# Performance work log

Measured on AMD Instinct MI355X. Metric: run time of the kernel, lower is better.

## Reference

```python
import jax, jax.numpy as jnp
import numpy as np

N_NODES = 50000
N_EDGES = 800000
D_FEAT = 128
D_EMB = 128


def setup_inputs() -> dict:
    key = jax.random.key(0)
    k1, k2, k3, k4, k5 = jax.random.split(key, 5)
    feature = jax.random.normal(k1, (N_NODES, D_FEAT), dtype=jnp.float32)
    edge_src = jax.random.randint(k2, (N_EDGES,), 0, N_NODES, dtype=jnp.int32)
    edge_dst = jax.random.randint(k3, (N_EDGES,), 0, N_NODES, dtype=jnp.int32)
    edge_w = jax.random.uniform(k4, (N_EDGES,), dtype=jnp.float32)
    # reset_parameters: uniform(-stdv, stdv), stdv = 1/sqrt(embedding_size)
    stdv = 1.0 / np.sqrt(D_EMB)
    weight = jax.random.uniform(k5, (D_FEAT, D_EMB), dtype=jnp.float32,
                                minval=-stdv, maxval=stdv)
    return {"feature": feature, "edge_src": edge_src, "edge_dst": edge_dst,
            "edge_w": edge_w, "weight": weight}


def reference(feature, edge_src, edge_dst, edge_w, weight):
    # spmm(adj, feature): out[dst] += w * feature[src]
    msgs = edge_w[:, None] * feature[edge_src]          # [E, D_FEAT]
    agg = jax.ops.segment_sum(msgs, edge_dst, num_segments=feature.shape[0])
    # residual blend then dense projection
    blended = 0.5 * agg + 0.5 * feature                  # [N, D_FEAT]
    return blended @ weight                              # [N, D_EMB]
```

## Files before the change

### kernel.cpp

```cpp
#include <hip/hip_runtime.h>

#define N_NODES 50000
#define N_EDGES 800000
#define D 128
#define NBUCK 196
#define CAP 4800
#define CHUNK 4096
#define PA_BLKS ((N_EDGES + CHUNK - 1) / CHUNK)
#define FB_BLKS 3125
#define WT_BLKS 16
#define GSTRIDE 16

typedef __attribute__((ext_vector_type(8))) short short8;
typedef __attribute__((ext_vector_type(4))) float f32x4;

__device__ __forceinline__ unsigned short f2bf(float f) {
    unsigned u = __float_as_uint(f);
    u += 0x7fff + ((u >> 16) & 1);
    return (unsigned short)(u >> 16);
}
__device__ __forceinline__ float lo16f(unsigned u) { return __uint_as_float(u << 16); }
__device__ __forceinline__ float hi16f(unsigned u) { return __uint_as_float(u & 0xffff0000u); }

__global__ __launch_bounds__(1024) void prep_passA(
    const float2* __restrict__ feat2, unsigned* __restrict__ fb,
    const float* __restrict__ W, unsigned short* __restrict__ Wt,
    const int* __restrict__ esrc, const int* __restrict__ edst,
    const float* __restrict__ ew, int* __restrict__ gcur,
    uint2* __restrict__ tmp) {
    __shared__ int lh[NBUCK], lbase[NBUCK], lcur[NBUCK];
    int blk = blockIdx.x, t = threadIdx.x;

    if (blk >= PA_BLKS) {
        int b2 = blk - PA_BLKS;
        if (b2 < FB_BLKS) {
            int i = b2 * 1024 + t;
            float2 f = feat2[i];
            fb[i] = (unsigned)f2bf(f.x) | ((unsigned)f2bf(f.y) << 16);
        } else {
            int idx = (b2 - FB_BLKS) * 1024 + t;
            int n = idx >> 7, k = idx & 127;
            Wt[idx] = f2bf(W[k * 128 + n]);
        }
        return;
    }

    for (int i = t; i < NBUCK; i += 1024) lh[i] = 0;
    __syncthreads();
    int e0 = blk * CHUNK;
    unsigned key[4];
    float wv[4];
#pragma unroll
    for (int j = 0; j < 4; ++j) {
        int e = e0 + j * 1024 + t;
        if (e < N_EDGES) {
            int src = esrc[e], dd = edst[e];
            key[j] = (unsigned)src | ((unsigned)(dd & 255) << 16) |
                     ((unsigned)(dd >> 8) << 24);
            wv[j] = ew[e];
            atomicAdd(&lh[dd >> 8], 1);
        } else key[j] = 0xff000000u;
    }
    __syncthreads();
    for (int i = t; i < NBUCK; i += 1024) {
        lbase[i] = atomicAdd(&gcur[i * GSTRIDE], lh[i]);
        lcur[i] = 0;
    }
    __syncthreads();
#pragma unroll
    for (int j = 0; j < 4; ++j) {
        int b = key[j] >> 24;
        if (b < NBUCK) {
            int r = atomicAdd(&lcur[b], 1);
            tmp[(size_t)b * CAP + lbase[b] + r] =
                make_uint2(key[j] & 0x00ffffffu, __float_as_uint(wv[j]));
        }
    }
}

__global__ __launch_bounds__(1024) void passB(const int* __restrict__ gcur,
                                              const uint2* __restrict__ tmp,
                                              int* __restrict__ offsets,
                                              uint2* __restrict__ sw) {
    __shared__ int hist[256], ps[256];
    int b = blockIdx.x, t = threadIdx.x;

    if (t < 256) ps[t] = (t < b) ? gcur[t * GSTRIDE] : 0;
    __syncthreads();
    for (int off = 128; off > 0; off >>= 1) {
        if (t < off) ps[t] += ps[t + off];
        __syncthreads();
    }
    int base = ps[0];
    int cnt = gcur[b * GSTRIDE];
    if (t < 256) hist[t] = 0;
    __syncthreads();

    const uint2* seg = tmp + (size_t)b * CAP;
    uint2 ent[5];
#pragma unroll
    for (int j = 0; j < 5; ++j) {
        int i = t + j * 1024;
        if (i < cnt) {
            ent[j] = seg[i];
            atomicAdd(&hist[ent[j].x >> 16], 1);
        }
    }
    __syncthreads();

    int h = 0;
    if (t < 256) { h = hist[t]; ps[t] = h; }
    __syncthreads();
    for (int off = 1; off < 256; off <<= 1) {
        int x = 0;
        if (t < 256 && t >= off) x = ps[t - off];
        __syncthreads();
        if (t < 256) ps[t] += x;
        __syncthreads();
    }
    int o = 0;
    if (t < 256) {
        o = base + ps[t] - h;
        int node = b * 256 + t;
        if (node < N_NODES) offsets[node] = o;
    }
    if (b == NBUCK - 1 && t == 0) offsets[N_NODES] = N_EDGES;
    __syncthreads();
    if (t < 256) hist[t] = o;
    __syncthreads();
#pragma unroll
    for (int j = 0; j < 5; ++j) {
        int i = t + j * 1024;
        if (i < cnt) {
            int pos = atomicAdd(&hist[ent[j].x >> 16], 1);
            sw[pos] = make_uint2(ent[j].x & 0xffffu, ent[j].y);
        }
    }
}

__global__ __launch_bounds__(256, 2) void agg_gemm(const int* __restrict__ offsets,
                                                   const uint2* __restrict__ sw,
                                                   const unsigned* __restrict__ fb,
                                                   const unsigned short* __restrict__ Wt,
                                                   float* __restrict__ out) {
    __shared__ unsigned Arows[16][68];
    int wave = threadIdx.x >> 6;
    int lane = threadIdx.x & 63;
    int row0 = blockIdx.x * 16;

#pragma unroll 1
    for (int i = 0; i < 4; ++i) {
        int n = __builtin_amdgcn_readfirstlane(row0 + wave * 4 + i);
        int b = offsets[n], e2 = offsets[n + 1];
        unsigned us = fb[(size_t)n * 64 + lane];
        float ax = 0.f, ay = 0.f;
        int e = b;
        int nfull = (e2 - b) >> 4;

        uint2 p[16];
        {
            int rem = e2 - e;
#pragma unroll
            for (int j = 0; j < 16; ++j) {
                int idx = (j < rem) ? j : (rem > 0 ? rem - 1 : 0);
                p[j] = sw[e + idx];
            }
        }
#pragma unroll 1
        for (int t = 0; t < nfull; ++t) {
            unsigned u[16];
#pragma unroll
            for (int j = 0; j < 16; ++j) u[j] = fb[(size_t)p[j].x * 64 + lane];
            int en = e + 16;
            int rem = e2 - en;
            uint2 pn[16];
#pragma unroll
            for (int j = 0; j < 16; ++j) {
                int idx = (j < rem) ? j : (rem > 0 ? rem - 1 : 0);
                pn[j] = sw[en + idx];
            }
#pragma unroll
            for (int j = 0; j < 16; ++j) {
                float w = __uint_as_float(p[j].y);
                ax += w * lo16f(u[j]);
                ay += w * hi16f(u[j]);
            }
#pragma unroll
            for (int j = 0; j < 16; ++j) p[j] = pn[j];
            e = en;
        }
        int rem = e2 - e;
        if (rem > 0) {
            unsigned u[16];
#pragma unroll
            for (int j = 0; j < 16; ++j) u[j] = fb[(size_t)p[j].x * 64 + lane];
#pragma unroll
            for (int j = 0; j < 16; ++j) {
                float w = (j < rem) ? __uint_as_float(p[j].y) : 0.f;
                ax += w * lo16f(u[j]);
                ay += w * hi16f(u[j]);
            }
        }
        float rx = 0.5f * (ax + lo16f(us));
        float ry = 0.5f * (ay + hi16f(us));
        Arows[wave * 4 + i][lane] = (unsigned)f2bf(rx) | ((unsigned)f2bf(ry) << 16);
    }
    __syncthreads();

    int quad = lane >> 4;
    int col  = lane & 15;
    short8 a[4];
#pragma unroll
    for (int kk = 0; kk < 4; ++kk)
        a[kk] = *reinterpret_cast<const short8*>(&Arows[col][kk * 16 + quad * 4]);

#pragma unroll
    for (int ii = 0; ii < 2; ++ii) {
        int n0 = wave * 2 + ii;
        const short8* bp = reinterpret_cast<const short8*>(Wt) + ((n0 * 16 + col) * 16 + quad);
        f32x4 acc = {0.f, 0.f, 0.f, 0.f};
        acc = __builtin_amdgcn_mfma_f32_16x16x32_bf16(a[0], bp[0],  acc, 0, 0, 0);
        acc = __builtin_amdgcn_mfma_f32_16x16x32_bf16(a[1], bp[4],  acc, 0, 0, 0);
        acc = __builtin_amdgcn_mfma_f32_16x16x32_bf16(a[2], bp[8],  acc, 0, 0, 0);
        acc = __builtin_amdgcn_mfma_f32_16x16x32_bf16(a[3], bp[12], acc, 0, 0, 0);
#pragma unroll
        for (int rr = 0; rr < 4; ++rr)
            out[(size_t)(row0 + quad * 4 + rr) * D + n0 * 16 + col] = acc[rr];
    }
}

extern "C" void kernel_launch(void* const* d_in, const int* in_sizes, int n_in,
                              void* d_out, int out_size, void* d_ws, size_t ws_size,
                              hipStream_t stream) {
    const float* feat = (const float*)d_in[0];
    const int*   esrc = (const int*)d_in[1];
    const int*   edst = (const int*)d_in[2];
    const float* ew   = (const float*)d_in[3];
    const float* W    = (const float*)d_in[4];
    float*       out  = (float*)d_out;

    char* ws = (char*)d_ws;
    uint2*          sw      = (uint2*)(ws + 0);
    unsigned*       fb      = (unsigned*)(ws + 6400000);
    int*            offsets = (int*)(ws + 19200000);
    unsigned short* Wt      = (unsigned short*)(ws + 19400064);
    int*            gcur    = (int*)(ws + 19432832);
    uint2* tmp = (uint2*)d_out;

    hipMemsetAsync(gcur, 0, NBUCK * GSTRIDE * sizeof(int), stream);
    prep_passA<<<PA_BLKS + FB_BLKS + WT_BLKS, 1024, 0, stream>>>(
        (const float2*)feat, fb, W, Wt, esrc, edst, ew, gcur, tmp);
    passB<<<NBUCK, 1024, 0, stream>>>(gcur, tmp, offsets, sw);
    agg_gemm<<<N_NODES / 16, 256, 0, stream>>>(offsets, sw, fb, Wt, out);
}
```

Before: 147.4 us.

## Split wave into two half-waves gathering separate edges with 8-byte loads

The aggregation loop now has each half of the 64-lane wave handle a different edge. Each lane loads 4 bf16 features (uint2) instead of 2, so one wave processes 32 edges per iteration with 16 wider gather loads. Partial sums from the two halves are combined with a cross-lane xor shuffle before the residual blend. The explicit prefetch of the next edge batch into a separate register array is dropped: the next 32 edges load after the FMAs, which may reduce latency hiding. The change also raises register pressure through the 32-entry edge array.

```diff
diff --git a/kernel.cpp b/kernel.cpp
--- a/kernel.cpp
+++ b/kernel.cpp
@@ -146,64 +146,76 @@
     __shared__ unsigned Arows[16][68];
     int wave = threadIdx.x >> 6;
     int lane = threadIdx.x & 63;
+    int half = lane >> 5;
+    int li   = lane & 31;
     int row0 = blockIdx.x * 16;
 
 #pragma unroll 1
     for (int i = 0; i < 4; ++i) {
         int n = __builtin_amdgcn_readfirstlane(row0 + wave * 4 + i);
         int b = offsets[n], e2 = offsets[n + 1];
-        unsigned us = fb[(size_t)n * 64 + lane];
-        float ax = 0.f, ay = 0.f;
+        float a0 = 0.f, a1 = 0.f, a2 = 0.f, a3 = 0.f;
         int e = b;
-        int nfull = (e2 - b) >> 4;
-
-        uint2 p[16];
+        int nfull = (e2 - b) >> 5;
+
+        uint2 p[32];
         {
             int rem = e2 - e;
 #pragma unroll
-            for (int j = 0; j < 16; ++j) {
+            for (int j = 0; j < 32; ++j) {
                 int idx = (j < rem) ? j : (rem > 0 ? rem - 1 : 0);
                 p[j] = sw[e + idx];
             }
         }
 #pragma unroll 1
         for (int t = 0; t < nfull; ++t) {
-            unsigned u[16];
-#pragma unroll
-            for (int j = 0; j < 16; ++j) u[j] = fb[(size_t)p[j].x * 64 + lane];
-            int en = e + 16;
-            int rem = e2 - en;
-            uint2 pn[16];
-#pragma unroll
-            for (int j = 0; j < 16; ++j) {
+            uint2 u[16];
+#pragma unroll
+            for (int k = 0; k < 16; ++k) {
+                unsigned s = half ? p[2 * k + 1].x : p[2 * k].x;
+                u[k] = *reinterpret_cast<const uint2*>(fb + (size_t)s * 64 + li * 2);
+            }
+#pragma unroll
+            for (int k = 0; k < 16; ++k) {
+                float w = __uint_as_float(half ? p[2 * k + 1].y : p[2 * k].y);
+                a0 += w * lo16f(u[k].x); a1 += w * hi16f(u[k].x);
+                a2 += w * lo16f(u[k].y); a3 += w * hi16f(u[k].y);
+            }
+            e += 32;
+            int rem = e2 - e;
+#pragma unroll
+            for (int j = 0; j < 32; ++j) {
                 int idx = (j < rem) ? j : (rem > 0 ? rem - 1 : 0);
-                pn[j] = sw[en + idx];
-            }
-#pragma unroll
-            for (int j = 0; j < 16; ++j) {
-                float w = __uint_as_float(p[j].y);
-                ax += w * lo16f(u[j]);
-                ay += w * hi16f(u[j]);
-            }
-#pragma unroll
-            for (int j = 0; j < 16; ++j) p[j] = pn[j];
-            e = en;
+                p[j] = sw[e + idx];
+            }
         }
         int rem = e2 - e;
         if (rem > 0) {
-            unsigned u[16];
-#pragma unroll
-            for (int j = 0; j < 16; ++j) u[j] = fb[(size_t)p[j].x * 64 + lane];
-#pragma unroll
-            for (int j = 0; j < 16; ++j) {
-                float w = (j < rem) ? __uint_as_float(p[j].y) : 0.f;
-                ax += w * lo16f(u[j]);
-                ay += w * hi16f(u[j]);
-            }
-        }
+            uint2 u[16];
+#pragma unroll
+            for (int k = 0; k < 16; ++k) {
+                unsigned s = half ? p[2 * k + 1].x : p[2 * k].x;
+                u[k] = *reinterpret_cast<const uint2*>(fb + (size_t)s * 64 + li * 2);
+            }
+#pragma unroll
+            for (int k = 0; k < 16; ++k) {
+                int jj = 2 * k + half;
+                float w = (jj < rem)
+                              ? __uint_as_float(half ? p[2 * k + 1].y : p[2 * k].y)
+                              : 0.f;
+                a0 += w * lo16f(u[k].x); a1 += w * hi16f(u[k].x);
+                a2 += w * lo16f(u[k].y); a3 += w * hi16f(u[k].y);
+            }
+        }
+        a0 += __shfl_xor(a0, 32); a1 += __shfl_xor(a1, 32);
+        a2 += __shfl_xor(a2, 32); a3 += __shfl_xor(a3, 32);
+        float ax = half ? a2 : a0;
+        float ay = half ? a3 : a1;
+        unsigned us = fb[(size_t)n * 64 + li * 2 + half];
         float rx = 0.5f * (ax + lo16f(us));
         float ry = 0.5f * (ay + hi16f(us));
-        Arows[wave * 4 + i][lane] = (unsigned)f2bf(rx) | ((unsigned)f2bf(ry) << 16);
+        Arows[wave * 4 + i][li * 2 + half] =
+            (unsigned)f2bf(rx) | ((unsigned)f2bf(ry) << 16);
     }
     __syncthreads();
 
```

Result: slower. 313.9 us (+112.9%).
